# Performance work log

Hardware: AMD Instinct MI355X
Metric: run time of the kernel (lower is better)

Reference implementation:

```python
import jax, jax.numpy as jnp
import numpy as np

N = 100_000      # num nodes
E = 100_000      # num hyperedges
NNZ = 1_600_000  # incidence entries (avg degree 16)
DIN = 128
DOUT = 128


def setup_inputs() -> dict:
    key = jax.random.key(0)
    k1, k2, k3, k4 = jax.random.split(key, 4)
    x = jax.random.normal(k1, (N, DIN), dtype=jnp.float32)
    weight = jax.random.normal(k2, (DIN, DOUT), dtype=jnp.float32) / np.sqrt(DIN).astype(np.float32)
    bias = jax.random.normal(k3, (DOUT,), dtype=jnp.float32) * 0.02
    hyperedge_index = jax.random.randint(k4, (2, NNZ), 0, N, dtype=jnp.int64)
    return {"x": x, "weight": weight, "bias": bias, "hyperedge_index": hyperedge_index}


def reference(x, weight, bias, hyperedge_index):
    # PyG HypergraphConv (use_attention=False, heads=1):
    #   out = D^{-1} H W B^{-1} H^T (x @ Theta) + bias, W = I (unit hyperedge weights)
    node_idx = hyperedge_index[0]  # [NNZ]
    edge_idx = hyperedge_index[1]  # [NNZ]

    h = x @ weight  # [N, DOUT]

    ones = jnp.ones((NNZ,), dtype=h.dtype)
    # node degree D_i = sum of hyperedge weights (=1) over incident hyperedges
    D = jax.ops.segment_sum(ones, node_idx, num_segments=N)   # [N]
    # hyperedge degree B_e = number of incident nodes
    B = jax.ops.segment_sum(ones, edge_idx, num_segments=E)   # [E]
    Dinv = jnp.where(D > 0, 1.0 / D, 0.0)
    Binv = jnp.where(B > 0, 1.0 / B, 0.0)

    # nodes -> hyperedges: m_e = B_e^{-1} * sum_{i in e} h_i
    e_feat = jax.ops.segment_sum(h[node_idx], edge_idx, num_segments=E) * Binv[:, None]  # [E, DOUT]
    # hyperedges -> nodes: out_i = D_i^{-1} * sum_{e ni i} m_e
    out = jax.ops.segment_sum(e_feat[edge_idx], node_idx, num_segments=N) * Dinv[:, None]  # [N, DOUT]
    return out + bias
```

## Files before the change

kernel.cpp:

```cpp
#include <hip/hip_runtime.h>

#define Nn 100000
#define Ne 100000
#define NNZC 1600000
#define NBLK 256
#define CHUNK 6250
#define BSH 8
#define BUCKW 256
#define NBK 391

typedef __attribute__((ext_vector_type(8))) short short8;
typedef __attribute__((ext_vector_type(4))) float floatx4;

__device__ inline unsigned short f2bf(float f) {
    union { float f; unsigned int i; } c; c.f = f;
    unsigned int i = c.i;
    return (unsigned short)((i + 0x7fffu + ((i >> 16) & 1u)) >> 16);
}
__device__ inline unsigned int f2bf2(float lo, float hi) {
    union { float f; unsigned int i; } a, b;
    a.f = lo; b.f = hi;
    const unsigned int x = (a.i + 0x7fffu + ((a.i >> 16) & 1u)) >> 16;
    const unsigned int y = (b.i + 0x7fffu + ((b.i >> 16) & 1u)) & 0xffff0000u;
    return x | y;
}

__global__ void hist_kernel(const int* __restrict__ nidx, const int* __restrict__ eidx,
                            int* __restrict__ histN, int* __restrict__ histE) {
    __shared__ int hN[NBK], hE[NBK];
    for (int j = threadIdx.x; j < NBK; j += 256) { hN[j] = 0; hE[j] = 0; }
    __syncthreads();
    const int base = blockIdx.x * CHUNK;
    for (int i = base + threadIdx.x; i < base + CHUNK; i += 256) {
        atomicAdd(&hN[nidx[i] >> BSH], 1);
        atomicAdd(&hE[eidx[i] >> BSH], 1);
    }
    __syncthreads();
    for (int j = threadIdx.x; j < NBK; j += 256) {
        histN[j * NBLK + blockIdx.x] = hN[j];
        histE[j * NBLK + blockIdx.x] = hE[j];
    }
}

__global__ void scan1_kernel(int* __restrict__ histN, int* __restrict__ histE,
                             int* __restrict__ bsumN, int* __restrict__ bsumE) {
    const int arr = blockIdx.x / NBK;
    const int b = blockIdx.x % NBK;
    int* a = arr ? histE : histN;
    int* bs = arr ? bsumE : bsumN;
    const int t = threadIdx.x;
    int v = a[b * 256 + t];
    __shared__ int tmp[2][256];
    int pin = 0;
    tmp[0][t] = v;
    for (int off = 1; off < 256; off <<= 1) {
        __syncthreads();
        int val = tmp[pin][t];
        if (t >= off) val += tmp[pin][t - off];
        tmp[1 - pin][t] = val;
        pin ^= 1;
    }
    __syncthreads();
    int incl = tmp[pin][t];
    a[b * 256 + t] = incl - v;
    if (t == 255) bs[b] = incl;
}

__global__ void scan3_kernel(int* __restrict__ histN, int* __restrict__ histE,
                             const int* __restrict__ bsumN, const int* __restrict__ bsumE) {
    const int arr = blockIdx.x / NBK;
    const int b = blockIdx.x % NBK;
    int* a = arr ? histE : histN;
    const int* bs = arr ? bsumE : bsumN;
    const int t = threadIdx.x;
    int part = 0;
    for (int i = t; i < b; i += 256) part += bs[i];
    __shared__ int red[256];
    red[t] = part;
    __syncthreads();
    for (int off = 128; off > 0; off >>= 1) {
        if (t < off) red[t] += red[t + off];
        __syncthreads();
    }
    a[b * 256 + t] += red[0];
}

__global__ void scatter_kernel(const int* __restrict__ nidx, const int* __restrict__ eidx,
                               const int* __restrict__ histN, const int* __restrict__ histE,
                               unsigned int* __restrict__ pairsN, unsigned int* __restrict__ pairsE) {
    __shared__ int cN[NBK], cE[NBK];
    const int blk = blockIdx.x;
    for (int j = threadIdx.x; j < NBK; j += 256) {
        cN[j] = histN[j * NBLK + blk];
        cE[j] = histE[j * NBLK + blk];
    }
    __syncthreads();
    const int base = blk * CHUNK;
    for (int i = base + threadIdx.x; i < base + CHUNK; i += 256) {
        const int n = nidx[i], e = eidx[i];
        const int pn = atomicAdd(&cN[n >> BSH], 1);
        const int pe = atomicAdd(&cE[e >> BSH], 1);
        pairsN[pn] = ((unsigned int)e << 8) | (unsigned int)(n & 255);
        pairsE[pe] = ((unsigned int)n << 8) | (unsigned int)(e & 255);
    }
}

__global__ void fine_kernel(const unsigned int* __restrict__ pairsN, const unsigned int* __restrict__ pairsE,
                            const int* __restrict__ histN, const int* __restrict__ histE,
                            int* __restrict__ offsN, int* __restrict__ offsE,
                            int* __restrict__ permN, int* __restrict__ permE) {
    const int arr = blockIdx.x / NBK;
    const int b = blockIdx.x % NBK;
    const unsigned int* pairs = arr ? pairsE : pairsN;
    const int* hist = arr ? histE : histN;
    int* offs = arr ? offsE : offsN;
    int* perm = arr ? permE : permN;
    const int t = threadIdx.x;
    const int S = hist[b * NBLK];
    const int E = (b + 1 < NBK) ? hist[(b + 1) * NBLK] : NNZC;
    __shared__ int cnt[BUCKW];
    __shared__ int tmp[2][BUCKW];
    cnt[t] = 0;
    __syncthreads();
    for (int i = S + t; i < E; i += BUCKW)
        atomicAdd(&cnt[pairs[i] & 255u], 1);
    __syncthreads();
    int v = cnt[t];
    int pin = 0;
    tmp[0][t] = v;
    for (int off = 1; off < BUCKW; off <<= 1) {
        __syncthreads();
        int val = tmp[pin][t];
        if (t >= off) val += tmp[pin][t - off];
        tmp[1 - pin][t] = val;
        pin ^= 1;
    }
    __syncthreads();
    const int excl = tmp[pin][t] - v;
    const int id = b * BUCKW + t;
    if (id < 100000) offs[id] = S + excl;
    if (b == NBK - 1 && t == 0) offs[100000] = NNZC;
    __syncthreads();
    cnt[t] = excl;
    __syncthreads();
    for (int i = S + t; i < E; i += BUCKW) {
        const unsigned int p = pairs[i];
        const int pos = S + atomicAdd(&cnt[p & 255u], 1);
        perm[pos] = (int)(p >> 8);
    }
}

__global__ __launch_bounds__(256) void gemm_mfma_kernel(const float* __restrict__ x,
                                                        const float* __restrict__ w,
                                                        unsigned short* __restrict__ h) {
    __shared__ unsigned short wlds[128 * 136];
    __shared__ unsigned short tile[4][16 * 136];
    const int tid = threadIdx.x;
    const int wave = tid >> 6, lane = tid & 63;
    const int q = lane >> 4, r16 = lane & 15;

    for (int i = tid; i < 4096; i += 256) {
        const int k = i >> 5;
        const int n0 = (i & 31) << 2;
        const float4 wv = *(const float4*)(w + k * 128 + n0);
        wlds[(n0 + 0) * 136 + k] = f2bf(wv.x);
        wlds[(n0 + 1) * 136 + k] = f2bf(wv.y);
        wlds[(n0 + 2) * 136 + k] = f2bf(wv.z);
        wlds[(n0 + 3) * 136 + k] = f2bf(wv.w);
    }
    __syncthreads();

    const int row0 = blockIdx.x * 64 + wave * 16;
    if (row0 >= Nn) return;

    floatx4 acc[8];
#pragma unroll
    for (int jb = 0; jb < 8; ++jb) acc[jb] = (floatx4){0.f, 0.f, 0.f, 0.f};

    const float* ap = x + (size_t)(row0 + r16) * 128 + q * 8;
#pragma unroll
    for (int kk = 0; kk < 4; ++kk) {
        const float4 a0 = *(const float4*)(ap + kk * 32);
        const float4 a1 = *(const float4*)(ap + kk * 32 + 4);
        union { unsigned int u[4]; short8 s; } af;
        af.u[0] = f2bf2(a0.x, a0.y);
        af.u[1] = f2bf2(a0.z, a0.w);
        af.u[2] = f2bf2(a1.x, a1.y);
        af.u[3] = f2bf2(a1.z, a1.w);
        const unsigned short* wp = wlds + kk * 32 + q * 8;
#pragma unroll
        for (int jb = 0; jb < 8; ++jb) {
            const short8 bfr = *(const short8*)(wp + (jb * 16 + r16) * 136);
            acc[jb] = __builtin_amdgcn_mfma_f32_16x16x32_bf16(af.s, bfr, acc[jb], 0, 0, 0);
        }
    }

    unsigned short* tw = tile[wave];
#pragma unroll
    for (int jb = 0; jb < 8; ++jb)
#pragma unroll
        for (int r = 0; r < 4; ++r)
            tw[(q * 4 + r) * 136 + jb * 16 + r16] = f2bf(acc[jb][r]);

    const int rr = lane >> 2, seg = lane & 3;
    const unsigned short* src = tw + rr * 136 + seg * 32;
    unsigned short* dst = h + (size_t)(row0 + rr) * 128 + seg * 32;
    *(short8*)(dst + 0)  = *(const short8*)(src + 0);
    *(short8*)(dst + 8)  = *(const short8*)(src + 8);
    *(short8*)(dst + 16) = *(const short8*)(src + 16);
    *(short8*)(dst + 24) = *(const short8*)(src + 24);
}

__device__ inline void gather_rows(const char* __restrict__ src, const int* __restrict__ perm,
                                   int start, int end, int lane, float& ax, float& ay) {
    const unsigned int laneoff = (unsigned int)lane << 2;
    for (int s0 = start; s0 < end; s0 += 64) {
        const int m = min(end - s0, 64);
        const int myv = perm[s0 + (lane < m ? lane : 0)];
        int t = 0;
        for (; t + 3 < m; t += 4) {
            const unsigned int a0 = ((unsigned int)__shfl(myv, t, 64) << 8) | laneoff;
            const unsigned int a1 = ((unsigned int)__shfl(myv, t + 1, 64) << 8) | laneoff;
            const unsigned int a2 = ((unsigned int)__shfl(myv, t + 2, 64) << 8) | laneoff;
            const unsigned int a3 = ((unsigned int)__shfl(myv, t + 3, 64) << 8) | laneoff;
            const unsigned int u0 = *(const unsigned int*)(src + a0);
            const unsigned int u1 = *(const unsigned int*)(src + a1);
            const unsigned int u2 = *(const unsigned int*)(src + a2);
            const unsigned int u3 = *(const unsigned int*)(src + a3);
            ax += __uint_as_float(u0 << 16); ay += __uint_as_float(u0 & 0xffff0000u);
            ax += __uint_as_float(u1 << 16); ay += __uint_as_float(u1 & 0xffff0000u);
            ax += __uint_as_float(u2 << 16); ay += __uint_as_float(u2 & 0xffff0000u);
            ax += __uint_as_float(u3 << 16); ay += __uint_as_float(u3 & 0xffff0000u);
        }
        for (; t < m; ++t) {
            const unsigned int a0 = ((unsigned int)__shfl(myv, t, 64) << 8) | laneoff;
            const unsigned int u0 = *(const unsigned int*)(src + a0);
            ax += __uint_as_float(u0 << 16); ay += __uint_as_float(u0 & 0xffff0000u);
        }
    }
}

__global__ void gather_n2e_kernel(const int* __restrict__ perm, const int* __restrict__ offs,
                                  const unsigned short* __restrict__ h,
                                  unsigned short* __restrict__ ef) {
    const int wave = threadIdx.x >> 6;
    const int lane = threadIdx.x & 63;
    const int e = blockIdx.x * 4 + wave;
    const int start = offs[e], end = offs[e + 1];
    float ax = 0.f, ay = 0.f;
    gather_rows((const char*)h, perm, start, end, lane, ax, ay);
    const int deg = end - start;
    const float binv = deg ? 1.f / (float)deg : 0.f;
    const unsigned int o = f2bf2(ax * binv, ay * binv);
    *(unsigned int*)((char*)ef + (((unsigned int)e << 8) | ((unsigned int)lane << 2))) = o;
}

__global__ void gather_e2n_kernel(const int* __restrict__ perm, const int* __restrict__ offs,
                                  const unsigned short* __restrict__ ef,
                                  const float* __restrict__ bias,
                                  float* __restrict__ out) {
    const int wave = threadIdx.x >> 6;
    const int lane = threadIdx.x & 63;
    const int n = blockIdx.x * 4 + wave;
    const int start = offs[n], end = offs[n + 1];
    float ax = 0.f, ay = 0.f;
    gather_rows((const char*)ef, perm, start, end, lane, ax, ay);
    const int deg = end - start;
    const float dinv = deg ? 1.f / (float)deg : 0.f;
    const float2 b = ((const float2*)bias)[lane];
    float2 o;
    o.x = ax * dinv + b.x;
    o.y = ay * dinv + b.y;
    *(float2*)((char*)out + (((unsigned int)n << 9) | ((unsigned int)lane << 3))) = o;
}

extern "C" void kernel_launch(void* const* d_in, const int* in_sizes, int n_in,
                              void* d_out, int out_size, void* d_ws, size_t ws_size,
                              hipStream_t stream) {
    const float* x = (const float*)d_in[0];
    const float* w = (const float*)d_in[1];
    const float* bias = (const float*)d_in[2];
    const int* hei = (const int*)d_in[3];
    const int* nidx = hei;
    const int* eidx = hei + NNZC;
    float* out = (float*)d_out;

    char* p = (char*)d_ws;
    unsigned short* h = (unsigned short*)p;  p += (size_t)Nn * 128 * 2;
    unsigned short* ef = (unsigned short*)p; p += (size_t)Ne * 128 * 2;
    int* histN = (int*)p;                    p += (size_t)NBK * NBLK * 4 + 256;
    int* histE = (int*)p;                    p += (size_t)NBK * NBLK * 4 + 256;
    int* bsumN = (int*)p;                    p += 1792;
    int* bsumE = (int*)p;                    p += 1792;
    int* offsN = (int*)p;                    p += 400128;
    int* offsE = (int*)p;                    p += 400128;
    int* permN = (int*)p;                    p += (size_t)NNZC * 4;
    int* permE = (int*)p;                    p += (size_t)NNZC * 4;
    unsigned int* pairsN = (unsigned int*)p; p += (size_t)NNZC * 4;
    unsigned int* pairsE = (unsigned int*)p; p += (size_t)NNZC * 4;

    gemm_mfma_kernel<<<(Nn + 63) / 64, 256, 0, stream>>>(x, w, h);

    hist_kernel<<<NBLK, 256, 0, stream>>>(nidx, eidx, histN, histE);
    scan1_kernel<<<2 * NBK, 256, 0, stream>>>(histN, histE, bsumN, bsumE);
    scan3_kernel<<<2 * NBK, 256, 0, stream>>>(histN, histE, bsumN, bsumE);
    scatter_kernel<<<NBLK, 256, 0, stream>>>(nidx, eidx, histN, histE, pairsN, pairsE);
    fine_kernel<<<2 * NBK, BUCKW, 0, stream>>>(pairsN, pairsE, histN, histE,
                                               offsN, offsE, permN, permE);

    gather_n2e_kernel<<<Ne / 4, 256, 0, stream>>>(permE, offsE, h, ef);
    gather_e2n_kernel<<<Nn / 4, 256, 0, stream>>>(permN, offsN, ef, bias, out);
}
```

Baseline: 320.9 us.

## Merge GEMM and scatter into one launch and unroll gather by eight

The separate GEMM and scatter kernels become one launch. Block IDs pick either the MFMA GEMM path or the CSR scatter path, and the shared memory of the two paths is overlaid with a union. This removes one launch and lets the independent GEMM and scatter work run at the same time on the device. Separately, the gather loop is unrolled from 4 to 8 loads in flight, with a masked tail in place of the scalar remainder loop. The cost is more registers and extra masked loads in the tail. The union sizes LDS for the larger GEMM path, which may reduce occupancy for the scatter blocks.

```diff
diff --git a/kernel.cpp b/kernel.cpp
--- a/kernel.cpp
+++ b/kernel.cpp
@@ -8,6 +8,7 @@
 #define BSH 8
 #define BUCKW 256
 #define NBK 391
+#define GEMM_BLOCKS 1563
 
 typedef __attribute__((ext_vector_type(8))) short short8;
 typedef __attribute__((ext_vector_type(4))) float floatx4;
@@ -85,23 +86,87 @@
     a[b * 256 + t] += red[0];
 }
 
-__global__ void scatter_kernel(const int* __restrict__ nidx, const int* __restrict__ eidx,
-                               const int* __restrict__ histN, const int* __restrict__ histE,
-                               unsigned int* __restrict__ pairsN, unsigned int* __restrict__ pairsE) {
-    __shared__ int cN[NBK], cE[NBK];
-    const int blk = blockIdx.x;
-    for (int j = threadIdx.x; j < NBK; j += 256) {
-        cN[j] = histN[j * NBLK + blk];
-        cE[j] = histE[j * NBLK + blk];
-    }
-    __syncthreads();
-    const int base = blk * CHUNK;
-    for (int i = base + threadIdx.x; i < base + CHUNK; i += 256) {
-        const int n = nidx[i], e = eidx[i];
-        const int pn = atomicAdd(&cN[n >> BSH], 1);
-        const int pe = atomicAdd(&cE[e >> BSH], 1);
-        pairsN[pn] = ((unsigned int)e << 8) | (unsigned int)(n & 255);
-        pairsE[pe] = ((unsigned int)n << 8) | (unsigned int)(e & 255);
+__global__ __launch_bounds__(256) void gemm_scatter_kernel(
+        const float* __restrict__ x, const float* __restrict__ w,
+        unsigned short* __restrict__ h,
+        const int* __restrict__ nidx, const int* __restrict__ eidx,
+        const int* __restrict__ histN, const int* __restrict__ histE,
+        unsigned int* __restrict__ pairsN, unsigned int* __restrict__ pairsE) {
+    __shared__ union {
+        struct { unsigned short wlds[128 * 136]; unsigned short tile[4][16 * 136]; } g;
+        struct { int cN[NBK]; int cE[NBK]; } s;
+    } sm;
+    const int tid = threadIdx.x;
+
+    if (blockIdx.x < GEMM_BLOCKS) {
+        const int wave = tid >> 6, lane = tid & 63;
+        const int q = lane >> 4, r16 = lane & 15;
+
+        for (int i = tid; i < 4096; i += 256) {
+            const int k = i >> 5;
+            const int n0 = (i & 31) << 2;
+            const float4 wv = *(const float4*)(w + k * 128 + n0);
+            sm.g.wlds[(n0 + 0) * 136 + k] = f2bf(wv.x);
+            sm.g.wlds[(n0 + 1) * 136 + k] = f2bf(wv.y);
+            sm.g.wlds[(n0 + 2) * 136 + k] = f2bf(wv.z);
+            sm.g.wlds[(n0 + 3) * 136 + k] = f2bf(wv.w);
+        }
+        __syncthreads();
+
+        const int row0 = blockIdx.x * 64 + wave * 16;
+        if (row0 >= Nn) return;
+
+        floatx4 acc[8];
+#pragma unroll
+        for (int jb = 0; jb < 8; ++jb) acc[jb] = (floatx4){0.f, 0.f, 0.f, 0.f};
+
+        const float* ap = x + (size_t)(row0 + r16) * 128 + q * 8;
+#pragma unroll
+        for (int kk = 0; kk < 4; ++kk) {
+            const float4 a0 = *(const float4*)(ap + kk * 32);
+            const float4 a1 = *(const float4*)(ap + kk * 32 + 4);
+            union { unsigned int u[4]; short8 s; } af;
+            af.u[0] = f2bf2(a0.x, a0.y);
+            af.u[1] = f2bf2(a0.z, a0.w);
+            af.u[2] = f2bf2(a1.x, a1.y);
+            af.u[3] = f2bf2(a1.z, a1.w);
+            const unsigned short* wp = sm.g.wlds + kk * 32 + q * 8;
+#pragma unroll
+            for (int jb = 0; jb < 8; ++jb) {
+                const short8 bfr = *(const short8*)(wp + (jb * 16 + r16) * 136);
+                acc[jb] = __builtin_amdgcn_mfma_f32_16x16x32_bf16(af.s, bfr, acc[jb], 0, 0, 0);
+            }
+        }
+
+        unsigned short* tw = sm.g.tile[wave];
+#pragma unroll
+        for (int jb = 0; jb < 8; ++jb)
+#pragma unroll
+            for (int r = 0; r < 4; ++r)
+                tw[(q * 4 + r) * 136 + jb * 16 + r16] = f2bf(acc[jb][r]);
+
+        const int rr = lane >> 2, seg = lane & 3;
+        const unsigned short* src = tw + rr * 136 + seg * 32;
+        unsigned short* dst = h + (size_t)(row0 + rr) * 128 + seg * 32;
+        *(short8*)(dst + 0)  = *(const short8*)(src + 0);
+        *(short8*)(dst + 8)  = *(const short8*)(src + 8);
+        *(short8*)(dst + 16) = *(const short8*)(src + 16);
+        *(short8*)(dst + 24) = *(const short8*)(src + 24);
+    } else {
+        const int blk = blockIdx.x - GEMM_BLOCKS;
+        for (int j = tid; j < NBK; j += 256) {
+            sm.s.cN[j] = histN[j * NBLK + blk];
+            sm.s.cE[j] = histE[j * NBLK + blk];
+        }
+        __syncthreads();
+        const int base = blk * CHUNK;
+        for (int i = base + tid; i < base + CHUNK; i += 256) {
+            const int n = nidx[i], e = eidx[i];
+            const int pn = atomicAdd(&sm.s.cN[n >> BSH], 1);
+            const int pe = atomicAdd(&sm.s.cE[e >> BSH], 1);
+            pairsN[pn] = ((unsigned int)e << 8) | (unsigned int)(n & 255);
+            pairsE[pe] = ((unsigned int)n << 8) | (unsigned int)(e & 255);
+        }
     }
 }
 
@@ -150,67 +215,6 @@
     }
 }
 
-__global__ __launch_bounds__(256) void gemm_mfma_kernel(const float* __restrict__ x,
-                                                        const float* __restrict__ w,
-                                                        unsigned short* __restrict__ h) {
-    __shared__ unsigned short wlds[128 * 136];
-    __shared__ unsigned short tile[4][16 * 136];
-    const int tid = threadIdx.x;
-    const int wave = tid >> 6, lane = tid & 63;
-    const int q = lane >> 4, r16 = lane & 15;
-
-    for (int i = tid; i < 4096; i += 256) {
-        const int k = i >> 5;
-        const int n0 = (i & 31) << 2;
-        const float4 wv = *(const float4*)(w + k * 128 + n0);
-        wlds[(n0 + 0) * 136 + k] = f2bf(wv.x);
-        wlds[(n0 + 1) * 136 + k] = f2bf(wv.y);
-        wlds[(n0 + 2) * 136 + k] = f2bf(wv.z);
-        wlds[(n0 + 3) * 136 + k] = f2bf(wv.w);
-    }
-    __syncthreads();
-
-    const int row0 = blockIdx.x * 64 + wave * 16;
-    if (row0 >= Nn) return;
-
-    floatx4 acc[8];
-#pragma unroll
-    for (int jb = 0; jb < 8; ++jb) acc[jb] = (floatx4){0.f, 0.f, 0.f, 0.f};
-
-    const float* ap = x + (size_t)(row0 + r16) * 128 + q * 8;
-#pragma unroll
-    for (int kk = 0; kk < 4; ++kk) {
-        const float4 a0 = *(const float4*)(ap + kk * 32);
-        const float4 a1 = *(const float4*)(ap + kk * 32 + 4);
-        union { unsigned int u[4]; short8 s; } af;
-        af.u[0] = f2bf2(a0.x, a0.y);
-        af.u[1] = f2bf2(a0.z, a0.w);
-        af.u[2] = f2bf2(a1.x, a1.y);
-        af.u[3] = f2bf2(a1.z, a1.w);
-        const unsigned short* wp = wlds + kk * 32 + q * 8;
-#pragma unroll
-        for (int jb = 0; jb < 8; ++jb) {
-            const short8 bfr = *(const short8*)(wp + (jb * 16 + r16) * 136);
-            acc[jb] = __builtin_amdgcn_mfma_f32_16x16x32_bf16(af.s, bfr, acc[jb], 0, 0, 0);
-        }
-    }
-
-    unsigned short* tw = tile[wave];
-#pragma unroll
-    for (int jb = 0; jb < 8; ++jb)
-#pragma unroll
-        for (int r = 0; r < 4; ++r)
-            tw[(q * 4 + r) * 136 + jb * 16 + r16] = f2bf(acc[jb][r]);
-
-    const int rr = lane >> 2, seg = lane & 3;
-    const unsigned short* src = tw + rr * 136 + seg * 32;
-    unsigned short* dst = h + (size_t)(row0 + rr) * 128 + seg * 32;
-    *(short8*)(dst + 0)  = *(const short8*)(src + 0);
-    *(short8*)(dst + 8)  = *(const short8*)(src + 8);
-    *(short8*)(dst + 16) = *(const short8*)(src + 16);
-    *(short8*)(dst + 24) = *(const short8*)(src + 24);
-}
-
 __device__ inline void gather_rows(const char* __restrict__ src, const int* __restrict__ perm,
                                    int start, int end, int lane, float& ax, float& ay) {
     const unsigned int laneoff = (unsigned int)lane << 2;
@@ -218,24 +222,35 @@
         const int m = min(end - s0, 64);
         const int myv = perm[s0 + (lane < m ? lane : 0)];
         int t = 0;
-        for (; t + 3 < m; t += 4) {
-            const unsigned int a0 = ((unsigned int)__shfl(myv, t, 64) << 8) | laneoff;
-            const unsigned int a1 = ((unsigned int)__shfl(myv, t + 1, 64) << 8) | laneoff;
-            const unsigned int a2 = ((unsigned int)__shfl(myv, t + 2, 64) << 8) | laneoff;
-            const unsigned int a3 = ((unsigned int)__shfl(myv, t + 3, 64) << 8) | laneoff;
-            const unsigned int u0 = *(const unsigned int*)(src + a0);
-            const unsigned int u1 = *(const unsigned int*)(src + a1);
-            const unsigned int u2 = *(const unsigned int*)(src + a2);
-            const unsigned int u3 = *(const unsigned int*)(src + a3);
-            ax += __uint_as_float(u0 << 16); ay += __uint_as_float(u0 & 0xffff0000u);
-            ax += __uint_as_float(u1 << 16); ay += __uint_as_float(u1 & 0xffff0000u);
-            ax += __uint_as_float(u2 << 16); ay += __uint_as_float(u2 & 0xffff0000u);
-            ax += __uint_as_float(u3 << 16); ay += __uint_as_float(u3 & 0xffff0000u);
-        }
-        for (; t < m; ++t) {
-            const unsigned int a0 = ((unsigned int)__shfl(myv, t, 64) << 8) | laneoff;
-            const unsigned int u0 = *(const unsigned int*)(src + a0);
-            ax += __uint_as_float(u0 << 16); ay += __uint_as_float(u0 & 0xffff0000u);
+        for (; t + 7 < m; t += 8) {
+            unsigned int a[8], u[8];
+#pragma unroll
+            for (int j = 0; j < 8; ++j)
+                a[j] = ((unsigned int)__shfl(myv, t + j, 64) << 8) | laneoff;
+#pragma unroll
+            for (int j = 0; j < 8; ++j) u[j] = *(const unsigned int*)(src + a[j]);
+#pragma unroll
+            for (int j = 0; j < 8; ++j) {
+                ax += __uint_as_float(u[j] << 16);
+                ay += __uint_as_float(u[j] & 0xffff0000u);
+            }
+        }
+        if (t < m) {
+            unsigned int a[8], u[8];
+            float f[8];
+#pragma unroll
+            for (int j = 0; j < 8; ++j) {
+                const int idx = (t + j < m) ? t + j : t;
+                f[j] = (t + j < m) ? 1.f : 0.f;
+                a[j] = ((unsigned int)__shfl(myv, idx, 64) << 8) | laneoff;
+            }
+#pragma unroll
+            for (int j = 0; j < 8; ++j) u[j] = *(const unsigned int*)(src + a[j]);
+#pragma unroll
+            for (int j = 0; j < 8; ++j) {
+                ax += f[j] * __uint_as_float(u[j] << 16);
+                ay += f[j] * __uint_as_float(u[j] & 0xffff0000u);
+            }
         }
     }
 }
@@ -299,12 +314,11 @@
     unsigned int* pairsN = (unsigned int*)p; p += (size_t)NNZC * 4;
     unsigned int* pairsE = (unsigned int*)p; p += (size_t)NNZC * 4;
 
-    gemm_mfma_kernel<<<(Nn + 63) / 64, 256, 0, stream>>>(x, w, h);
-
     hist_kernel<<<NBLK, 256, 0, stream>>>(nidx, eidx, histN, histE);
     scan1_kernel<<<2 * NBK, 256, 0, stream>>>(histN, histE, bsumN, bsumE);
     scan3_kernel<<<2 * NBK, 256, 0, stream>>>(histN, histE, bsumN, bsumE);
-    scatter_kernel<<<NBLK, 256, 0, stream>>>(nidx, eidx, histN, histE, pairsN, pairsE);
+    gemm_scatter_kernel<<<GEMM_BLOCKS + NBLK, 256, 0, stream>>>(
+        x, w, h, nidx, eidx, histN, histE, pairsN, pairsE);
     fine_kernel<<<2 * NBK, BUCKW, 0, stream>>>(pairsN, pairsE, histN, histE,
                                                offsN, offsE, permN, permE);
 
```

After: 313.1 us. 2.4% less time.
